# Kernel tuning notes

Measured on AMD Instinct MI355X. Metric: run time of the kernel, lower is better.

## Reference

```python
import jax, jax.numpy as jnp
import numpy as np


def _mlp2(x, W1, b1, W2, b2):
    # two-layer MLP with ReLU hidden activation
    h = jax.nn.relu(jnp.einsum('...i,ij->...j', x, W1) + b1)
    return jnp.einsum('...i,ij->...j', h, W2) + b2


def setup_inputs() -> dict:
    key = jax.random.key(0)
    ks = jax.random.split(key, 8)
    B, N, D = 8, 256, 64
    positions = jax.random.normal(ks[0], (B, N, 3), dtype=jnp.float32)
    values = jax.random.normal(ks[1], (B, N, D), dtype=jnp.float32)
    # value_net: 2 -> D -> D ; score_net: D -> D -> 1 (He-style init)
    Wv1 = jax.random.normal(ks[2], (2, D), dtype=jnp.float32) * np.sqrt(2.0 / 2)
    bv1 = jnp.zeros((D,), dtype=jnp.float32)
    Wv2 = jax.random.normal(ks[3], (D, D), dtype=jnp.float32) * np.sqrt(2.0 / D)
    bv2 = jnp.zeros((D,), dtype=jnp.float32)
    Ws1 = jax.random.normal(ks[4], (D, D), dtype=jnp.float32) * np.sqrt(2.0 / D)
    bs1 = jnp.zeros((D,), dtype=jnp.float32)
    Ws2 = jax.random.normal(ks[5], (D, 1), dtype=jnp.float32) * np.sqrt(2.0 / D)
    bs2 = jnp.zeros((1,), dtype=jnp.float32)
    return dict(positions=positions, values=values, Wv1=Wv1, bv1=bv1, Wv2=Wv2,
                bv2=bv2, Ws1=Ws1, bs1=bs1, Ws2=Ws2, bs2=bs2)


def reference(positions, values, Wv1, bv1, Wv2, bv2, Ws1, bs1, Ws2, bs2):
    # rank-2 geometric algebra attention, reduce=True, merge_fun=join_fun='mean'
    B, N, _ = positions.shape
    r_i = positions[:, :, None, :]            # [B, N, 1, 3]
    r_j = positions[:, None, :, :]            # [B, 1, N, 3]
    # geometric product of two vectors -> scalar (dot) + bivector (wedge)
    dot = jnp.sum(r_i * r_j, axis=-1)         # [B, N, N] scalar part
    wedge = jnp.cross(r_i, r_j)               # [B, N, N, 3] bivector components
    biv_norm = jnp.sqrt(jnp.sum(wedge * wedge, axis=-1) + 1e-20)
    invariants = jnp.stack([dot, biv_norm], axis=-1)             # [B, N, N, 2]
    # merge_fun='mean' over the pair of node values
    merged = 0.5 * (values[:, :, None, :] + values[:, None, :, :])  # [B,N,N,D]
    invar_values = _mlp2(invariants, Wv1, bv1, Wv2, bv2)            # [B,N,N,D]
    # join_fun='mean' of value_net(invariants) and merged node values
    joined = 0.5 * (invar_values + merged)                          # [B,N,N,D]
    scores = _mlp2(joined, Ws1, bs1, Ws2, bs2)                      # [B,N,N,1]
    # reduce=True: softmax over all N*N product indices, output is [B, D]
    attn = jax.nn.softmax(scores.reshape(B, N * N), axis=-1).reshape(B, N, N, 1)
    output = jnp.sum(attn * joined, axis=(1, 2))                    # [B, D]
    return output
```

## Files before the change

kernel.cpp:

```cpp
#include <hip/hip_runtime.h>
#include <hip/hip_bf16.h>

#define NB 8
#define NN 256
#define DD 64

#define OFF_WCSW  0
#define OFF_CSA   2048
#define OFF_CSB   3072
#define OFF_CSC   4096
#define OFF_CC    5120
#define OFF_M     5184
#define OFF_RS    5248
#define OFF_U     7296
#define OFF_SC    138368

typedef __attribute__((ext_vector_type(4))) float f32x4;
typedef __attribute__((ext_vector_type(8))) short s16x8;

static __device__ __forceinline__ unsigned short bf16_rn(float x) {
    unsigned u = __float_as_uint(x);
    u += 0x8000u;
    return (unsigned short)(u >> 16);
}

__global__ __launch_bounds__(256) void k_setup(
    const float* __restrict__ values, const float* __restrict__ Wv1,
    const float* __restrict__ bv1, const float* __restrict__ Wv2,
    const float* __restrict__ bv2, const float* __restrict__ Ws1,
    const float* __restrict__ bs1, float* __restrict__ ws)
{
    int idx = blockIdx.x * 256 + threadIdx.x;
    if (idx < 131072) {
        int d = idx & 63;
        const float* v = values + (idx >> 6) * 64;
        float s = 0.f;
        for (int k = 0; k < 64; k++) s = fmaf(v[k], Ws1[k * 64 + d], s);
        ws[OFF_U + idx] = 0.25f * s;
    } else if (idx < 135168) {
        int e = idx - 131072;
        int j = e & 7, lane = (e >> 3) & 63, nt = (e >> 9) & 3, ks = e >> 11;
        int k = ks * 32 + ((lane >> 4) & 3) * 8 + j;
        int d = nt * 16 + (lane & 15);
        float s = 0.f;
        for (int m = 0; m < 64; m++) s = fmaf(Wv2[k * 64 + m], Ws1[m * 64 + d], s);
        ((unsigned short*)(ws + OFF_WCSW))[e] = bf16_rn(0.5f * s);
    } else if (idx < 136192) {
        int e = idx - 135168;
        int j = e & 7, lane = (e >> 3) & 63, ks = e >> 9;
        int k = ks * 32 + ((lane >> 4) & 3) * 8 + j;
        ws[OFF_CSA + e] = Wv1[k];
        ws[OFF_CSB + e] = Wv1[64 + k];
        ws[OFF_CSC + e] = bv1[k];
    } else if (idx < 136256) {
        int d = idx - 136192;
        float s = 0.f;
        for (int k = 0; k < 64; k++) s = fmaf(bv2[k], Ws1[k * 64 + d], s);
        ws[OFF_CC + d] = 0.5f * s + bs1[d];
    } else if (idx < 136264) {
        ((unsigned*)(ws + OFF_M))[idx - 136256] = 0u;
    }
}

__global__ __launch_bounds__(256, 2) void k_pass1(
    const float* __restrict__ pos, const float* __restrict__ Ws2,
    float* __restrict__ ws)
{
    __shared__ float2 ldsDB[2 * 256];
    __shared__ float  ldsCCU[2 * 64];
    __shared__ float  ldsWs2[64];
    __shared__ float  ldsPos[6];
    __shared__ float  ldsRed[256];

    int b  = blockIdx.x >> 7;
    int i0 = (blockIdx.x & 127) * 2;
    int t  = threadIdx.x;
    const float* uB = ws + OFF_U + b * (NN * DD);

    if (t < 6)  ldsPos[t] = pos[(b * 256 + i0) * 3 + t];
    if (t < 64) ldsWs2[t] = Ws2[t];
    if (t < 128) {
        int ii = t >> 6, d = t & 63;
        ldsCCU[t] = ws[OFF_CC + d] + uB[(i0 + ii) * 64 + d];
    }
    __syncthreads();

    {
        float px = pos[(b * 256 + t) * 3 + 0];
        float py = pos[(b * 256 + t) * 3 + 1];
        float pz = pos[(b * 256 + t) * 3 + 2];
#pragma unroll
        for (int ii = 0; ii < 2; ii++) {
            float ax = ldsPos[ii * 3 + 0], ay = ldsPos[ii * 3 + 1], az = ldsPos[ii * 3 + 2];
            float dot = ax * px + ay * py + az * pz;
            float cx = ay * pz - az * py;
            float cy = az * px - ax * pz;
            float cz = ax * py - ay * px;
            float biv = sqrtf(cx * cx + cy * cy + cz * cz + 1e-20f);
            ldsDB[ii * 256 + t] = make_float2(dot, biv);
        }
    }
    __syncthreads();

    int lane = t & 63, w = t >> 6;
    int q = lane >> 4, col = lane & 15;

    float cA[16], cB[16], cC[16];
    {
        const f32x4* pa0 = (const f32x4*)(ws + OFF_CSA + lane * 8);
        const f32x4* pa1 = (const f32x4*)(ws + OFF_CSA + 512 + lane * 8);
        ((f32x4*)cA)[0] = pa0[0]; ((f32x4*)cA)[1] = pa0[1];
        ((f32x4*)cA)[2] = pa1[0]; ((f32x4*)cA)[3] = pa1[1];
        const f32x4* pb0 = (const f32x4*)(ws + OFF_CSB + lane * 8);
        const f32x4* pb1 = (const f32x4*)(ws + OFF_CSB + 512 + lane * 8);
        ((f32x4*)cB)[0] = pb0[0]; ((f32x4*)cB)[1] = pb0[1];
        ((f32x4*)cB)[2] = pb1[0]; ((f32x4*)cB)[3] = pb1[1];
        const f32x4* pc0 = (const f32x4*)(ws + OFF_CSC + lane * 8);
        const f32x4* pc1 = (const f32x4*)(ws + OFF_CSC + 512 + lane * 8);
        ((f32x4*)cC)[0] = pc0[0]; ((f32x4*)cC)[1] = pc0[1];
        ((f32x4*)cC)[2] = pc1[0]; ((f32x4*)cC)[3] = pc1[1];
    }

    s16x8 bf[2][4];
    {
        const s16x8* wsw = (const s16x8*)(ws + OFF_WCSW);
#pragma unroll
        for (int ks = 0; ks < 2; ks++)
#pragma unroll
            for (int nt = 0; nt < 4; nt++)
                bf[ks][nt] = wsw[(ks * 4 + nt) * 64 + lane];
    }

    float wmax = -3.4e38f;
    float* scrow_base = ws + OFF_SC + (b * 256 + i0) * 256;

#pragma unroll
    for (int jt4 = 0; jt4 < 4; jt4++) {
        int jt = w * 4 + jt4;
        float uc[4][4];
#pragma unroll
        for (int r = 0; r < 4; r++) {
            int jl = jt * 16 + q * 4 + r;
#pragma unroll
            for (int nt = 0; nt < 4; nt++)
                uc[r][nt] = uB[jl * 64 + nt * 16 + col];
        }
#pragma unroll
        for (int ii = 0; ii < 2; ii++) {
            float2 db = ldsDB[ii * 256 + jt * 16 + col];
            s16x8 af[2];
#pragma unroll
            for (int ks = 0; ks < 2; ks++)
#pragma unroll
                for (int j = 0; j < 8; j++) {
                    float h = fmaf(db.x, cA[ks * 8 + j], fmaf(db.y, cB[ks * 8 + j], cC[ks * 8 + j]));
                    af[ks][j] = (short)bf16_rn(fmaxf(h, 0.f));
                }
            f32x4 acc[4];
#pragma unroll
            for (int nt = 0; nt < 4; nt++) acc[nt] = (f32x4){0.f, 0.f, 0.f, 0.f};
#pragma unroll
            for (int nt = 0; nt < 4; nt++) {
                acc[nt] = __builtin_amdgcn_mfma_f32_16x16x32_bf16(af[0], bf[0][nt], acc[nt], 0, 0, 0);
                acc[nt] = __builtin_amdgcn_mfma_f32_16x16x32_bf16(af[1], bf[1][nt], acc[nt], 0, 0, 0);
            }
            float tr[4] = {0.f, 0.f, 0.f, 0.f};
#pragma unroll
            for (int nt = 0; nt < 4; nt++) {
                float cu = ldsCCU[ii * 64 + nt * 16 + col];
                float w2 = ldsWs2[nt * 16 + col];
#pragma unroll
                for (int r = 0; r < 4; r++) {
                    float s = acc[nt][r] + cu + uc[r][nt];
                    tr[r] = fmaf(fmaxf(s, 0.f), w2, tr[r]);
                }
            }
#pragma unroll
            for (int m = 1; m < 16; m <<= 1) {
#pragma unroll
                for (int r = 0; r < 4; r++) tr[r] += __shfl_xor(tr[r], m);
            }
            wmax = fmaxf(wmax, fmaxf(fmaxf(tr[0], tr[1]), fmaxf(tr[2], tr[3])));
            if (col == 0) {
                float4 sc4 = make_float4(tr[0], tr[1], tr[2], tr[3]);
                *(float4*)(scrow_base + ii * 256 + jt * 16 + q * 4) = sc4;
            }
        }
    }

    ldsRed[t] = wmax;
    __syncthreads();
    for (int off = 128; off > 0; off >>= 1) {
        if (t < off) ldsRed[t] = fmaxf(ldsRed[t], ldsRed[t + off]);
        __syncthreads();
    }
    if (t == 0) {
        unsigned bits = __float_as_uint(ldsRed[0]);
        unsigned key = (bits & 0x80000000u) ? ~bits : (bits | 0x80000000u);
        atomicMax((unsigned*)(ws + OFF_M) + b, key);
    }
}

__global__ __launch_bounds__(256) void k_pass2(
    const float* __restrict__ pos, const float* __restrict__ Wv1,
    const float* __restrict__ bv1, float* __restrict__ ws)
{
    __shared__ float  ldsW[256];
    __shared__ float2 ldsDB[256];
    __shared__ float  ldsP[4][64];
    __shared__ float  ldsRed[256];

    int b = blockIdx.x >> 8, i = blockIdx.x & 255;
    int t = threadIdx.x;

    unsigned key = ((const unsigned*)(ws + OFF_M))[b];
    unsigned mbits = (key & 0x80000000u) ? (key ^ 0x80000000u) : ~key;
    float m = __uint_as_float(mbits);

    float* srow = ws + OFF_SC + (b * 256 + i) * 256;
    float wgt = __expf(srow[t] - m);
    ldsW[t] = wgt;
    {
        float ax = pos[(b * 256 + i) * 3 + 0];
        float ay = pos[(b * 256 + i) * 3 + 1];
        float az = pos[(b * 256 + i) * 3 + 2];
        float px = pos[(b * 256 + t) * 3 + 0];
        float py = pos[(b * 256 + t) * 3 + 1];
        float pz = pos[(b * 256 + t) * 3 + 2];
        float dot = ax * px + ay * py + az * pz;
        float cx = ay * pz - az * py;
        float cy = az * px - ax * pz;
        float cz = ax * py - ay * px;
        float biv = sqrtf(cx * cx + cy * cy + cz * cz + 1e-20f);
        ldsDB[t] = make_float2(dot, biv);
    }
    ldsRed[t] = wgt;
    __syncthreads();
    for (int off = 128; off > 0; off >>= 1) {
        if (t < off) ldsRed[t] += ldsRed[t + off];
        __syncthreads();
    }
    if (t == 0) ws[OFF_RS + b * 256 + i] = ldsRed[0];

    int g = t >> 6, k = t & 63;
    float A = Wv1[k], B = Wv1[64 + k], C = bv1[k];
    float acc = 0.f;
#pragma unroll 4
    for (int jj = 0; jj < 64; jj++) {
        int j = g * 64 + jj;
        float2 db = ldsDB[j];
        float h = fmaxf(fmaf(db.x, A, fmaf(db.y, B, C)), 0.f);
        acc = fmaf(ldsW[j], h, acc);
    }
    ldsP[g][k] = acc;
    __syncthreads();
    if (t < 64) srow[t] = ldsP[0][t] + ldsP[1][t] + ldsP[2][t] + ldsP[3][t];
}

__global__ __launch_bounds__(256) void k_finalize(
    const float* __restrict__ values, const float* __restrict__ Wv2,
    const float* __restrict__ bv2, const float* __restrict__ ws,
    float* __restrict__ out)
{
    __shared__ float ldsRS[256], P1[4][64], P2[4][64], Sh[64];
    int b = blockIdx.x, t = threadIdx.x, g = t >> 6, x = t & 63;

    ldsRS[t] = ws[OFF_RS + b * 256 + t];
    const float* phb = ws + OFF_SC + b * (NN * NN);
    float shp = 0.f;
    for (int i = g * 64; i < g * 64 + 64; i++) shp += phb[i * 256 + x];
    P1[g][x] = shp;
    __syncthreads();
    if (t < 64) Sh[x] = P1[0][x] + P1[1][x] + P1[2][x] + P1[3][x];
    __syncthreads();

    float t1p = 0.f;
    for (int k = g * 16; k < g * 16 + 16; k++) t1p = fmaf(Sh[k], Wv2[k * 64 + x], t1p);
    float a2p = 0.f;
    const float* vb = values + b * (NN * DD);
    for (int i = g * 64; i < g * 64 + 64; i++) a2p = fmaf(ldsRS[i], vb[i * 64 + x], a2p);
    P1[g][x] = t1p; P2[g][x] = a2p;
    __syncthreads();

    if (t < 64) {
        float zp = ldsRS[x] + ldsRS[64 + x] + ldsRS[128 + x] + ldsRS[192 + x];
#pragma unroll
        for (int md = 32; md; md >>= 1) zp += __shfl_xor(zp, md);
        float t1 = P1[0][x] + P1[1][x] + P1[2][x] + P1[3][x];
        float a2 = P2[0][x] + P2[1][x] + P2[2][x] + P2[3][x];
        out[b * 64 + x] = 0.5f * (t1 + a2) / zp + 0.5f * bv2[x];
    }
}

extern "C" void kernel_launch(void* const* d_in, const int* in_sizes, int n_in,
                              void* d_out, int out_size, void* d_ws, size_t ws_size,
                              hipStream_t stream)
{
    const float* positions = (const float*)d_in[0];
    const float* values    = (const float*)d_in[1];
    const float* Wv1       = (const float*)d_in[2];
    const float* bv1       = (const float*)d_in[3];
    const float* Wv2       = (const float*)d_in[4];
    const float* bv2       = (const float*)d_in[5];
    const float* Ws1       = (const float*)d_in[6];
    const float* bs1       = (const float*)d_in[7];
    const float* Ws2       = (const float*)d_in[8];
    float* ws  = (float*)d_ws;
    float* out = (float*)d_out;

    k_setup<<<533, 256, 0, stream>>>(values, Wv1, bv1, Wv2, bv2, Ws1, bs1, ws);
    k_pass1<<<1024, 256, 0, stream>>>(positions, Ws2, ws);
    k_pass2<<<2048, 256, 0, stream>>>(positions, Wv1, bv1, ws);
    k_finalize<<<NB, 256, 0, stream>>>(values, Wv2, bv2, ws, out);
}
```

Before: 123.3 us.

## Fold final reductions into pass2 via atomics and shrink finalize kernel

Pass2 now pushes its per-row partial results (the weighted hidden sum, the row-weight-scaled values and the row sum) straight into per-batch accumulators with atomicAdd. This replaces the old finalize kernel, which ran only 8 blocks and serially re-read 256 rows per batch. A tiny k_out kernel then applies Wv2 and normalises. Block-level max and sum reductions also switch from LDS tree loops with repeated barriers to wavefront shuffles, and a few loops get unroll pragmas. The cost is atomic contention on 64 addresses per batch and fp32 summation order that is no longer deterministic.

```diff
diff --git a/kernel.cpp b/kernel.cpp
--- a/kernel.cpp
+++ b/kernel.cpp
@@ -11,7 +11,9 @@
 #define OFF_CSC   4096
 #define OFF_CC    5120
 #define OFF_M     5184
-#define OFF_RS    5248
+#define OFF_Z     5192
+#define OFF_SH    5200
+#define OFF_A2    5712
 #define OFF_U     7296
 #define OFF_SC    138368
 
@@ -35,6 +37,7 @@
         int d = idx & 63;
         const float* v = values + (idx >> 6) * 64;
         float s = 0.f;
+#pragma unroll 8
         for (int k = 0; k < 64; k++) s = fmaf(v[k], Ws1[k * 64 + d], s);
         ws[OFF_U + idx] = 0.25f * s;
     } else if (idx < 135168) {
@@ -43,6 +46,7 @@
         int k = ks * 32 + ((lane >> 4) & 3) * 8 + j;
         int d = nt * 16 + (lane & 15);
         float s = 0.f;
+#pragma unroll 8
         for (int m = 0; m < 64; m++) s = fmaf(Wv2[k * 64 + m], Ws1[m * 64 + d], s);
         ((unsigned short*)(ws + OFF_WCSW))[e] = bf16_rn(0.5f * s);
     } else if (idx < 136192) {
@@ -55,10 +59,17 @@
     } else if (idx < 136256) {
         int d = idx - 136192;
         float s = 0.f;
+#pragma unroll 8
         for (int k = 0; k < 64; k++) s = fmaf(bv2[k], Ws1[k * 64 + d], s);
         ws[OFF_CC + d] = 0.5f * s + bs1[d];
     } else if (idx < 136264) {
         ((unsigned*)(ws + OFF_M))[idx - 136256] = 0u;
+    } else if (idx < 136272) {
+        ws[OFF_Z + idx - 136264] = 0.f;
+    } else if (idx < 136784) {
+        ws[OFF_SH + idx - 136272] = 0.f;
+    } else if (idx < 137296) {
+        ws[OFF_A2 + idx - 136784] = 0.f;
     }
 }
 
@@ -188,14 +199,13 @@
         }
     }
 
-    ldsRed[t] = wmax;
-    __syncthreads();
-    for (int off = 128; off > 0; off >>= 1) {
-        if (t < off) ldsRed[t] = fmaxf(ldsRed[t], ldsRed[t + off]);
-        __syncthreads();
-    }
+#pragma unroll
+    for (int md = 1; md < 64; md <<= 1) wmax = fmaxf(wmax, __shfl_xor(wmax, md));
+    if (lane == 0) ldsRed[w] = wmax;
+    __syncthreads();
     if (t == 0) {
-        unsigned bits = __float_as_uint(ldsRed[0]);
+        float bm = fmaxf(fmaxf(ldsRed[0], ldsRed[1]), fmaxf(ldsRed[2], ldsRed[3]));
+        unsigned bits = __float_as_uint(bm);
         unsigned key = (bits & 0x80000000u) ? ~bits : (bits | 0x80000000u);
         atomicMax((unsigned*)(ws + OFF_M) + b, key);
     }
@@ -203,21 +213,22 @@
 
 __global__ __launch_bounds__(256) void k_pass2(
     const float* __restrict__ pos, const float* __restrict__ Wv1,
-    const float* __restrict__ bv1, float* __restrict__ ws)
+    const float* __restrict__ bv1, const float* __restrict__ values,
+    float* __restrict__ ws)
 {
     __shared__ float  ldsW[256];
     __shared__ float2 ldsDB[256];
     __shared__ float  ldsP[4][64];
-    __shared__ float  ldsRed[256];
+    __shared__ float  ldsR[4];
 
     int b = blockIdx.x >> 8, i = blockIdx.x & 255;
-    int t = threadIdx.x;
+    int t = threadIdx.x, w = t >> 6, lane = t & 63;
 
     unsigned key = ((const unsigned*)(ws + OFF_M))[b];
     unsigned mbits = (key & 0x80000000u) ? (key ^ 0x80000000u) : ~key;
     float m = __uint_as_float(mbits);
 
-    float* srow = ws + OFF_SC + (b * 256 + i) * 256;
+    const float* srow = ws + OFF_SC + (b * 256 + i) * 256;
     float wgt = __expf(srow[t] - m);
     ldsW[t] = wgt;
     {
@@ -234,62 +245,45 @@
         float biv = sqrtf(cx * cx + cy * cy + cz * cz + 1e-20f);
         ldsDB[t] = make_float2(dot, biv);
     }
-    ldsRed[t] = wgt;
-    __syncthreads();
-    for (int off = 128; off > 0; off >>= 1) {
-        if (t < off) ldsRed[t] += ldsRed[t + off];
-        __syncthreads();
-    }
-    if (t == 0) ws[OFF_RS + b * 256 + i] = ldsRed[0];
-
-    int g = t >> 6, k = t & 63;
-    float A = Wv1[k], B = Wv1[64 + k], C = bv1[k];
+    float r = wgt;
+#pragma unroll
+    for (int md = 1; md < 64; md <<= 1) r += __shfl_xor(r, md);
+    if (lane == 0) ldsR[w] = r;
+    __syncthreads();
+    float rs = ldsR[0] + ldsR[1] + ldsR[2] + ldsR[3];
+
+    float A = Wv1[lane], B = Wv1[64 + lane], C = bv1[lane];
     float acc = 0.f;
-#pragma unroll 4
+#pragma unroll 8
     for (int jj = 0; jj < 64; jj++) {
-        int j = g * 64 + jj;
+        int j = w * 64 + jj;
         float2 db = ldsDB[j];
         float h = fmaxf(fmaf(db.x, A, fmaf(db.y, B, C)), 0.f);
         acc = fmaf(ldsW[j], h, acc);
     }
-    ldsP[g][k] = acc;
-    __syncthreads();
-    if (t < 64) srow[t] = ldsP[0][t] + ldsP[1][t] + ldsP[2][t] + ldsP[3][t];
-}
-
-__global__ __launch_bounds__(256) void k_finalize(
-    const float* __restrict__ values, const float* __restrict__ Wv2,
-    const float* __restrict__ bv2, const float* __restrict__ ws,
-    float* __restrict__ out)
-{
-    __shared__ float ldsRS[256], P1[4][64], P2[4][64], Sh[64];
-    int b = blockIdx.x, t = threadIdx.x, g = t >> 6, x = t & 63;
-
-    ldsRS[t] = ws[OFF_RS + b * 256 + t];
-    const float* phb = ws + OFF_SC + b * (NN * NN);
-    float shp = 0.f;
-    for (int i = g * 64; i < g * 64 + 64; i++) shp += phb[i * 256 + x];
-    P1[g][x] = shp;
-    __syncthreads();
-    if (t < 64) Sh[x] = P1[0][x] + P1[1][x] + P1[2][x] + P1[3][x];
-    __syncthreads();
-
-    float t1p = 0.f;
-    for (int k = g * 16; k < g * 16 + 16; k++) t1p = fmaf(Sh[k], Wv2[k * 64 + x], t1p);
-    float a2p = 0.f;
-    const float* vb = values + b * (NN * DD);
-    for (int i = g * 64; i < g * 64 + 64; i++) a2p = fmaf(ldsRS[i], vb[i * 64 + x], a2p);
-    P1[g][x] = t1p; P2[g][x] = a2p;
-    __syncthreads();
-
+    ldsP[w][lane] = acc;
+    __syncthreads();
     if (t < 64) {
-        float zp = ldsRS[x] + ldsRS[64 + x] + ldsRS[128 + x] + ldsRS[192 + x];
-#pragma unroll
-        for (int md = 32; md; md >>= 1) zp += __shfl_xor(zp, md);
-        float t1 = P1[0][x] + P1[1][x] + P1[2][x] + P1[3][x];
-        float a2 = P2[0][x] + P2[1][x] + P2[2][x] + P2[3][x];
-        out[b * 64 + x] = 0.5f * (t1 + a2) / zp + 0.5f * bv2[x];
-    }
+        float sh = ldsP[0][t] + ldsP[1][t] + ldsP[2][t] + ldsP[3][t];
+        atomicAdd(ws + OFF_SH + b * 64 + t, sh);
+        atomicAdd(ws + OFF_A2 + b * 64 + t, rs * values[(b * 256 + i) * 64 + t]);
+    }
+    if (t == 0) atomicAdd(ws + OFF_Z + b, rs);
+}
+
+__global__ __launch_bounds__(64) void k_out(
+    const float* __restrict__ Wv2, const float* __restrict__ bv2,
+    const float* __restrict__ ws, float* __restrict__ out)
+{
+    __shared__ float sh[64];
+    int b = blockIdx.x, d = threadIdx.x;
+    sh[d] = ws[OFF_SH + b * 64 + d];
+    __syncthreads();
+    float t1 = 0.f;
+#pragma unroll 8
+    for (int k = 0; k < 64; k++) t1 = fmaf(sh[k], Wv2[k * 64 + d], t1);
+    float Z = ws[OFF_Z + b];
+    out[b * 64 + d] = 0.5f * (t1 + ws[OFF_A2 + b * 64 + d]) / Z + 0.5f * bv2[d];
 }
 
 extern "C" void kernel_launch(void* const* d_in, const int* in_sizes, int n_in,
@@ -308,8 +302,8 @@
     float* ws  = (float*)d_ws;
     float* out = (float*)d_out;
 
-    k_setup<<<533, 256, 0, stream>>>(values, Wv1, bv1, Wv2, bv2, Ws1, bs1, ws);
+    k_setup<<<537, 256, 0, stream>>>(values, Wv1, bv1, Wv2, bv2, Ws1, bs1, ws);
     k_pass1<<<1024, 256, 0, stream>>>(positions, Ws2, ws);
-    k_pass2<<<2048, 256, 0, stream>>>(positions, Wv1, bv1, ws);
-    k_finalize<<<NB, 256, 0, stream>>>(values, Wv2, bv2, ws, out);
-}
+    k_pass2<<<2048, 256, 0, stream>>>(positions, Wv1, bv1, values, ws);
+    k_out<<<NB, 64, 0, stream>>>(Wv2, bv2, ws, out);
+}
```

Result: slower. 132.7 us (+7.6%).
